# Kernel tuning notes

Hardware: AMD Instinct MI355X
Metric: run time of the kernel (lower is better)

The kernel has to match this reference:

```python
import jax, jax.numpy as jnp
import numpy as np

N, E, G = 50000, 800000, 200
F_IN, C, HEADS = 16, 64, 4
HID = C * HEADS  # 256


def setup_inputs() -> dict:
    key = jax.random.key(0)
    ks = jax.random.split(key, 30)
    rn = lambda k, s, sc=0.1: jax.random.normal(k, s, jnp.float32) * sc
    inp = {
        'x': jax.random.normal(ks[0], (N, F_IN), jnp.float32),
        'edge_index': jax.random.randint(ks[1], (2, E), 0, N, jnp.int32),
        'batch': jnp.sort(jax.random.randint(ks[2], (N,), 0, G, jnp.int32)),
        'Wl1': rn(ks[3], (F_IN, HID)), 'Wr1': rn(ks[4], (F_IN, HID)),
        'att1': rn(ks[5], (HEADS, C)), 'b1': rn(ks[6], (HID,)),
        'g1': jnp.ones((HID,), jnp.float32), 'be1': jnp.zeros((HID,), jnp.float32),
        'Wl2': rn(ks[7], (HID, HID)), 'Wr2': rn(ks[8], (HID, HID)),
        'att2': rn(ks[9], (HEADS, C)), 'b2': rn(ks[10], (HID,)),
        'g2': jnp.ones((HID,), jnp.float32), 'be2': jnp.zeros((HID,), jnp.float32),
        # GATv2 layer 3: 256 -> 64, 1 head, mean (concat=False)
        'Wl3': rn(ks[11], (HID, C)), 'Wr3': rn(ks[12], (HID, C)),
        'att3': rn(ks[13], (1, C)), 'b3': rn(ks[14], (C,)),
        'g3': jnp.ones((C,), jnp.float32), 'be3': jnp.zeros((C,), jnp.float32),
        # classifier MLP: 128 -> 64 -> 1
        'Wc1': rn(ks[15], (2 * C, C)), 'bc1': rn(ks[16], (C,)),
        'Wc2': rn(ks[17], (C, 1)), 'bc2': rn(ks[18], (1,)),
    }
    return inp


def _gatv2(x, src, dst, Wl, Wr, att, b, heads, c, concat):
    n = x.shape[0]
    xl = (x @ Wl).reshape(n, heads, c)
    xr = (x @ Wr).reshape(n, heads, c)
    s = jax.nn.leaky_relu(xl[src] + xr[dst], 0.2)       # [E', H, C]
    e = jnp.einsum('ehc,hc->eh', s, att)                 # [E', H]
    m = jax.ops.segment_max(e, dst, num_segments=n)
    p = jnp.exp(e - m[dst])
    denom = jax.ops.segment_sum(p, dst, num_segments=n)
    alpha = p / (denom[dst] + 1e-16)
    out = jax.ops.segment_sum(alpha[:, :, None] * xl[src], dst, num_segments=n)
    out = out.reshape(n, heads * c) if concat else out.mean(axis=1)
    return out + b


def _bn(x, g, b):
    mu = x.mean(0)
    v = x.var(0)
    return (x - mu) * jax.lax.rsqrt(v + 1e-5) * g + b


def reference(x, edge_index, batch,
              Wl1, Wr1, att1, b1, g1, be1,
              Wl2, Wr2, att2, b2, g2, be2,
              Wl3, Wr3, att3, b3, g3, be3,
              Wc1, bc1, Wc2, bc2):
    n = x.shape[0]
    loop = jnp.arange(n, dtype=edge_index.dtype)
    src = jnp.concatenate([edge_index[0], loop])  # PyG add_self_loops=True
    dst = jnp.concatenate([edge_index[1], loop])

    h = _gatv2(x, src, dst, Wl1, Wr1, att1, b1, HEADS, C, True)
    h = jax.nn.elu(_bn(h, g1, be1))  # dropout disabled (eval)
    h = _gatv2(h, src, dst, Wl2, Wr2, att2, b2, HEADS, C, True)
    h = jax.nn.elu(_bn(h, g2, be2))
    h = _gatv2(h, src, dst, Wl3, Wr3, att3, b3, 1, C, False)
    h = _bn(h, g3, be3)

    cnt = jax.ops.segment_sum(jnp.ones((n, 1), h.dtype), batch, num_segments=G)
    mean_pool = jax.ops.segment_sum(h, batch, num_segments=G) / jnp.maximum(cnt, 1.0)
    max_pool = jax.ops.segment_max(h, batch, num_segments=G)
    pooled = jnp.concatenate([mean_pool, max_pool], axis=1)  # [G, 128]

    out = jax.nn.relu(pooled @ Wc1 + bc1)
    out = out @ Wc2 + bc2  # [G, 1]
    return out
```

## Files before the change

kernel.cpp:

```cpp
#include <hip/hip_runtime.h>
#include <math.h>

#define N_NODES 50000
#define N_EDGES 800000
#define ET (N_EDGES + N_NODES)
#define N_GRAPHS 200
#define F_INN 16
#define C_DIM 64
#define N_HEADS 4
#define HIDD 256
#define SCAN_BLOCKS ((N_NODES + 255) / 256)

typedef __attribute__((ext_vector_type(8))) short short8;
typedef __attribute__((ext_vector_type(8))) ushort ushort8;
typedef __attribute__((ext_vector_type(4))) float f32x4;
typedef __attribute__((ext_vector_type(2))) float f32x2;

__device__ __forceinline__ float bf2f(ushort u) {
  return __uint_as_float(((unsigned)u) << 16);
}
__device__ __forceinline__ ushort f2bf(float f) {
  unsigned u = __float_as_uint(f);
  u += 0x7fff + ((u >> 16) & 1);
  return (ushort)(u >> 16);
}

__device__ __forceinline__ f32x2 emax2(f32x2 a, f32x2 b) {
#if __has_builtin(__builtin_elementwise_max)
  return __builtin_elementwise_max(a, b);
#else
  f32x2 r;
  r.x = fmaxf(a.x, b.x);
  r.y = fmaxf(a.y, b.y);
  return r;
#endif
}

template<int K, int M>
__global__ __launch_bounds__(256) void gemm_dual(
    const float* __restrict__ A, const float* __restrict__ Bl,
    const float* __restrict__ Br, ushort* __restrict__ Clb,
    ushort* __restrict__ Crb, int nrows)
{
  __shared__ __align__(16) float As[16][64];
  __shared__ __align__(16) float Bls[16][64];
  __shared__ __align__(16) float Brs[16][64];
  int tid = threadIdx.x;
  int row0 = blockIdx.x * 64;
  int col0 = blockIdx.y * 64;
  int tr = (tid >> 4) << 2;
  int tc = (tid & 15) << 2;
  float accL[4][4] = {{0.f}}, accR[4][4] = {{0.f}};
  int arow = tid >> 2, ak = (tid & 3) << 2;
  int brow = tid >> 4, bcol = (tid & 15) << 2;
  for (int k0 = 0; k0 < K; k0 += 16) {
    float4 av = make_float4(0.f, 0.f, 0.f, 0.f);
    int gr = row0 + arow;
    if (gr < nrows) av = *(const float4*)&A[(size_t)gr * K + k0 + ak];
    As[ak + 0][arow] = av.x;
    As[ak + 1][arow] = av.y;
    As[ak + 2][arow] = av.z;
    As[ak + 3][arow] = av.w;
    *(float4*)&Bls[brow][bcol] = *(const float4*)&Bl[(size_t)(k0 + brow) * M + col0 + bcol];
    *(float4*)&Brs[brow][bcol] = *(const float4*)&Br[(size_t)(k0 + brow) * M + col0 + bcol];
    __syncthreads();
    #pragma unroll
    for (int k = 0; k < 16; ++k) {
      float4 a = *(const float4*)&As[k][tr];
      float4 bl = *(const float4*)&Bls[k][tc];
      float4 br = *(const float4*)&Brs[k][tc];
      float aa[4] = {a.x, a.y, a.z, a.w};
      float lb[4] = {bl.x, bl.y, bl.z, bl.w};
      float rb[4] = {br.x, br.y, br.z, br.w};
      #pragma unroll
      for (int ii = 0; ii < 4; ++ii)
        #pragma unroll
        for (int jj = 0; jj < 4; ++jj) {
          accL[ii][jj] = fmaf(aa[ii], lb[jj], accL[ii][jj]);
          accR[ii][jj] = fmaf(aa[ii], rb[jj], accR[ii][jj]);
        }
    }
    __syncthreads();
  }
  #pragma unroll
  for (int ii = 0; ii < 4; ++ii) {
    int gr = row0 + tr + ii;
    if (gr < nrows) {
      *(ushort4*)&Clb[(size_t)gr * M + col0 + tc] =
          make_ushort4(f2bf(accL[ii][0]), f2bf(accL[ii][1]),
                       f2bf(accL[ii][2]), f2bf(accL[ii][3]));
      *(ushort4*)&Crb[(size_t)gr * M + col0 + tc] =
          make_ushort4(f2bf(accR[ii][0]), f2bf(accR[ii][1]),
                       f2bf(accR[ii][2]), f2bf(accR[ii][3]));
    }
  }
}

__device__ __forceinline__ void split_bf16(float a, ushort& hi, ushort& lo) {
  unsigned u = __float_as_uint(a);
  hi = (ushort)(u >> 16);
  float ah = __uint_as_float(u & 0xffff0000u);
  float r = a - ah;
  lo = (ushort)(__float_as_uint(r) >> 16);
}

template<int K, int N>
__global__ void convertB(const float* __restrict__ W, ushort* __restrict__ BTmat) {
  int idx = blockIdx.x * blockDim.x + threadIdx.x;
  if (idx >= K * N) return;
  int k = idx / N, n = idx - k * N;
  ushort hi, lo;
  split_bf16(W[idx], hi, lo);
  size_t dst = ((size_t)(k >> 3) * N + n) * 8 + (k & 7);
  BTmat[dst] = hi;
  BTmat[(size_t)(K / 8) * N * 8 + dst] = lo;
}

template<int N>
__global__ __launch_bounds__(N * 2) void gemm_fused(
    const float* __restrict__ H, const float* __restrict__ gsum,
    const float* __restrict__ gsumsq, const float* __restrict__ g,
    const float* __restrict__ be, const ushort* __restrict__ BT,
    ushort* __restrict__ Clb, ushort* __restrict__ Crb)
{
  constexpr int THREADS = N * 2;
  constexpr int PLANE = 32 * N * 8;
  __shared__ float SCs[256], SHs[256];
  __shared__ ushort Ah_s[64 * 256];
  __shared__ ushort Al_s[64 * 256];
  const int tid = threadIdx.x;
  const int brow0 = blockIdx.x * 64;

  const float invn = 1.0f / (float)N_NODES;
  for (int c = tid; c < 256; c += THREADS) {
    float mu = gsum[c] * invn;
    float var = gsumsq[c] * invn - mu * mu;
    float sc = g[c] * rsqrtf(var + 1e-5f);
    SCs[c] = sc;
    SHs[c] = be[c] - mu * sc;
  }
  __syncthreads();

  for (int gid = tid; gid < 2048; gid += THREADS) {
    int r = gid >> 5;
    int ch0 = (gid & 31) * 8;
    int grow = min(brow0 + r, N_NODES - 1);
    float4 v0 = *(const float4*)&H[(size_t)grow * 256 + ch0];
    float4 v1 = *(const float4*)&H[(size_t)grow * 256 + ch0 + 4];
    float4 sc0 = *(const float4*)&SCs[ch0];
    float4 sc1 = *(const float4*)&SCs[ch0 + 4];
    float4 sh0 = *(const float4*)&SHs[ch0];
    float4 sh1 = *(const float4*)&SHs[ch0 + 4];
    float vv[8] = {v0.x, v0.y, v0.z, v0.w, v1.x, v1.y, v1.z, v1.w};
    float scv[8] = {sc0.x, sc0.y, sc0.z, sc0.w, sc1.x, sc1.y, sc1.z, sc1.w};
    float shv[8] = {sh0.x, sh0.y, sh0.z, sh0.w, sh1.x, sh1.y, sh1.z, sh1.w};
    short8 hi8, lo8;
    #pragma unroll
    for (int j = 0; j < 8; ++j) {
      float t = fmaf(vv[j], scv[j], shv[j]);
      float e = t > 0.f ? t : __expf(t) - 1.f;
      ushort h, l;
      split_bf16(e, h, l);
      hi8[j] = (short)h;
      lo8[j] = (short)l;
    }
    int off = r * 512 + ((ch0 * 2) ^ ((r & 7) << 4));
    *(short8*)((char*)Ah_s + off) = hi8;
    *(short8*)((char*)Al_s + off) = lo8;
  }
  __syncthreads();

  const int wave = tid >> 6, lane = tid & 63;
  const int cn = lane & 15, kgrp = lane >> 4;
  const int combc = wave * 64;
  const bool isR = combc >= N;
  const ushort* Bh = BT + (isR ? 2 * PLANE : 0);
  const ushort* Bl_ = Bh + PLANE;
  const int cb = combc & (N - 1);
  f32x4 acc[4][4];
  #pragma unroll
  for (int rt = 0; rt < 4; ++rt)
    #pragma unroll
    for (int ct = 0; ct < 4; ++ct) acc[rt][ct] = (f32x4)(0.f);

  #pragma unroll 2
  for (int k0 = 0; k0 < 256; k0 += 32) {
    short8 ah[4], al[4];
    #pragma unroll
    for (int rt = 0; rt < 4; ++rt) {
      int row = rt * 16 + cn;
      int off = row * 512 + (((k0 * 2) + kgrp * 16) ^ ((row & 7) << 4));
      ah[rt] = *(const short8*)((const char*)Ah_s + off);
      al[rt] = *(const short8*)((const char*)Al_s + off);
    }
    const size_t bbase = (size_t)((k0 >> 3) + kgrp) * (N * 8);
    #pragma unroll
    for (int ct = 0; ct < 4; ++ct) {
      const size_t bo = bbase + (size_t)(cb + ct * 16 + cn) * 8;
      short8 bh = *(const short8*)&Bh[bo];
      short8 bl = *(const short8*)&Bl_[bo];
      #pragma unroll
      for (int rt = 0; rt < 4; ++rt) {
        acc[rt][ct] = __builtin_amdgcn_mfma_f32_16x16x32_bf16(ah[rt], bh, acc[rt][ct], 0, 0, 0);
        acc[rt][ct] = __builtin_amdgcn_mfma_f32_16x16x32_bf16(ah[rt], bl, acc[rt][ct], 0, 0, 0);
        acc[rt][ct] = __builtin_amdgcn_mfma_f32_16x16x32_bf16(al[rt], bh, acc[rt][ct], 0, 0, 0);
      }
    }
  }

  #pragma unroll
  for (int ct = 0; ct < 4; ++ct) {
    int cc = cb + ct * 16 + cn;
    #pragma unroll
    for (int rt = 0; rt < 4; ++rt) {
      int crow0 = brow0 + rt * 16 + kgrp * 4;
      #pragma unroll
      for (int j = 0; j < 4; ++j) {
        int rr = crow0 + j;
        if (rr < N_NODES) {
          if (!isR) Clb[(size_t)rr * N + cc] = f2bf(acc[rt][ct][j]);
          else      Crb[(size_t)rr * N + cc] = f2bf(acc[rt][ct][j]);
        }
      }
    }
  }
}

__global__ void hist_kernel(const int* __restrict__ dsts, int* __restrict__ curs) {
  int i = blockIdx.x * blockDim.x + threadIdx.x;
  if (i >= ET) return;
  int d = (i < N_EDGES) ? dsts[i] : i - N_EDGES;
  atomicAdd(&curs[d], 1);
}

__global__ __launch_bounds__(256) void scan_part(
    const int* __restrict__ curs, int* __restrict__ rows, int* __restrict__ bsum)
{
  __shared__ int tmp[256];
  int t = threadIdx.x;
  int i = blockIdx.x * 256 + t;
  int v = (i < N_NODES) ? curs[i] : 0;
  tmp[t] = v;
  __syncthreads();
  #pragma unroll
  for (int off = 1; off < 256; off <<= 1) {
    int u = (t >= off) ? tmp[t - off] : 0;
    __syncthreads();
    tmp[t] += u;
    __syncthreads();
  }
  if (i < N_NODES) rows[i] = tmp[t] - v;
  if (t == 255) bsum[blockIdx.x] = tmp[255];
}

__global__ __launch_bounds__(256) void scan_bsums(
    const int* __restrict__ bsum, int* __restrict__ boff)
{
  __shared__ int tmp[256];
  int t = threadIdx.x;
  int v = (t < SCAN_BLOCKS) ? bsum[t] : 0;
  tmp[t] = v;
  __syncthreads();
  #pragma unroll
  for (int off = 1; off < 256; off <<= 1) {
    int u = (t >= off) ? tmp[t - off] : 0;
    __syncthreads();
    tmp[t] += u;
    __syncthreads();
  }
  if (t < SCAN_BLOCKS) boff[t] = tmp[t] - v;
}

__global__ __launch_bounds__(256) void scan_apply(
    int* __restrict__ rows, const int* __restrict__ boff, int* __restrict__ curs)
{
  int i = blockIdx.x * 256 + threadIdx.x;
  if (i < N_NODES) {
    int r = rows[i] + boff[blockIdx.x];
    rows[i] = r;
    curs[i] = r;
  }
  if (i == 0) rows[N_NODES] = ET;
}

__global__ void scatter_kernel(const int* __restrict__ srcs, const int* __restrict__ dsts,
                               int* __restrict__ curs, int* __restrict__ esrc) {
  int i = blockIdx.x * blockDim.x + threadIdx.x;
  if (i >= ET) return;
  int s, d;
  if (i < N_EDGES) { s = srcs[i]; d = dsts[i]; } else { s = d = i - N_EDGES; }
  int pos = atomicAdd(&curs[d], 1);
  esrc[pos] = s;
}

__global__ __launch_bounds__(256) void flash256(
    const ushort* __restrict__ xl, const ushort* __restrict__ xr,
    const float* __restrict__ att, const int* __restrict__ rows,
    const int* __restrict__ esrc, float* __restrict__ out)
{
  int d = blockIdx.x * 4 + (threadIdx.x >> 6);
  if (d >= N_NODES) return;
  int lane = threadIdx.x & 63;
  int beg = rows[d], end = rows[d + 1];
  ushort4 ur = *(const ushort4*)&xr[(size_t)d * 256 + lane * 4];
  float xq0 = bf2f(ur.x), xq1 = bf2f(ur.y), xq2 = bf2f(ur.z), xq3 = bf2f(ur.w);
  float4 w = *(const float4*)&att[lane * 4];
  auto score = [&](float b0, float b1, float b2, float b3) {
    float v0 = b0 + xq0, v1 = b1 + xq1, v2 = b2 + xq2, v3 = b3 + xq3;
    v0 = v0 > 0.f ? v0 : 0.2f * v0;
    v1 = v1 > 0.f ? v1 : 0.2f * v1;
    v2 = v2 > 0.f ? v2 : 0.2f * v2;
    v3 = v3 > 0.f ? v3 : 0.2f * v3;
    return fmaf(v0, w.x, fmaf(v1, w.y, fmaf(v2, w.z, v3 * w.w)));
  };
  float m = -INFINITY, s = 0.f;
  float a0 = 0.f, a1 = 0.f, a2 = 0.f, a3 = 0.f;
  int p = beg;
  for (; p + 4 <= end; p += 4) {
    int s1 = esrc[p], s2 = esrc[p + 1], s3 = esrc[p + 2], s4 = esrc[p + 3];
    ushort4 u1 = *(const ushort4*)&xl[(size_t)s1 * 256 + lane * 4];
    ushort4 u2 = *(const ushort4*)&xl[(size_t)s2 * 256 + lane * 4];
    ushort4 u3 = *(const ushort4*)&xl[(size_t)s3 * 256 + lane * 4];
    ushort4 u4 = *(const ushort4*)&xl[(size_t)s4 * 256 + lane * 4];
    float b10 = bf2f(u1.x), b11 = bf2f(u1.y), b12 = bf2f(u1.z), b13 = bf2f(u1.w);
    float b20 = bf2f(u2.x), b21 = bf2f(u2.y), b22 = bf2f(u2.z), b23 = bf2f(u2.w);
    float b30 = bf2f(u3.x), b31 = bf2f(u3.y), b32 = bf2f(u3.z), b33 = bf2f(u3.w);
    float b40 = bf2f(u4.x), b41 = bf2f(u4.y), b42 = bf2f(u4.z), b43 = bf2f(u4.w);
    float e1 = score(b10, b11, b12, b13);
    float e2 = score(b20, b21, b22, b23);
    float e3 = score(b30, b31, b32, b33);
    float e4 = score(b40, b41, b42, b43);
    e1 += __shfl_xor(e1, 1); e2 += __shfl_xor(e2, 1);
    e3 += __shfl_xor(e3, 1); e4 += __shfl_xor(e4, 1);
    e1 += __shfl_xor(e1, 2); e2 += __shfl_xor(e2, 2);
    e3 += __shfl_xor(e3, 2); e4 += __shfl_xor(e4, 2);
    e1 += __shfl_xor(e1, 4); e2 += __shfl_xor(e2, 4);
    e3 += __shfl_xor(e3, 4); e4 += __shfl_xor(e4, 4);
    e1 += __shfl_xor(e1, 8); e2 += __shfl_xor(e2, 8);
    e3 += __shfl_xor(e3, 8); e4 += __shfl_xor(e4, 8);
    float mn = fmaxf(fmaxf(m, fmaxf(e1, e2)), fmaxf(e3, e4));
    float f = __expf(m - mn);
    float p1 = __expf(e1 - mn);
    float p2 = __expf(e2 - mn);
    float p3 = __expf(e3 - mn);
    float p4 = __expf(e4 - mn);
    s = s * f + ((p1 + p2) + (p3 + p4));
    a0 = fmaf(a0, f, fmaf(p1, b10, fmaf(p2, b20, fmaf(p3, b30, p4 * b40))));
    a1 = fmaf(a1, f, fmaf(p1, b11, fmaf(p2, b21, fmaf(p3, b31, p4 * b41))));
    a2 = fmaf(a2, f, fmaf(p1, b12, fmaf(p2, b22, fmaf(p3, b32, p4 * b42))));
    a3 = fmaf(a3, f, fmaf(p1, b13, fmaf(p2, b23, fmaf(p3, b33, p4 * b43))));
    m = mn;
  }
  for (; p < end; ++p) {
    int s1 = esrc[p];
    ushort4 u1 = *(const ushort4*)&xl[(size_t)s1 * 256 + lane * 4];
    float b10 = bf2f(u1.x), b11 = bf2f(u1.y), b12 = bf2f(u1.z), b13 = bf2f(u1.w);
    float e1 = score(b10, b11, b12, b13);
    e1 += __shfl_xor(e1, 1);
    e1 += __shfl_xor(e1, 2);
    e1 += __shfl_xor(e1, 4);
    e1 += __shfl_xor(e1, 8);
    float mn = fmaxf(m, e1);
    float f = __expf(m - mn);
    float p1 = __expf(e1 - mn);
    s = fmaf(s, f, p1);
    a0 = fmaf(a0, f, p1 * b10);
    a1 = fmaf(a1, f, p1 * b11);
    a2 = fmaf(a2, f, p1 * b12);
    a3 = fmaf(a3, f, p1 * b13);
    m = mn;
  }
  float inv = 1.f / (s + 1e-16f);
  *(float4*)&out[(size_t)d * 256 + lane * 4] =
      make_float4(a0 * inv, a1 * inv, a2 * inv, a3 * inv);
}

__global__ __launch_bounds__(256) void flash64(
    const ushort* __restrict__ xl, const ushort* __restrict__ xr,
    const float* __restrict__ att, const int* __restrict__ rows,
    const int* __restrict__ esrc, float* __restrict__ out)
{
  const int wave = threadIdx.x >> 6, lane = threadIdx.x & 63;
  const int di = lane >> 3, sl = lane & 7;
  const int d = blockIdx.x * 32 + wave * 8 + di;
  const bool valid = d < N_NODES;
  const int dc = valid ? d : N_NODES - 1;
  const int ch = sl * 8;
  ushort8 uxr = *(const ushort8*)&xr[(size_t)dc * 64 + ch];
  float4 wa = *(const float4*)&att[ch];
  float4 wb = *(const float4*)&att[ch + 4];
  f32x2 xr0 = {bf2f(uxr[0]), bf2f(uxr[1])}, xr1 = {bf2f(uxr[2]), bf2f(uxr[3])};
  f32x2 xr2 = {bf2f(uxr[4]), bf2f(uxr[5])}, xr3 = {bf2f(uxr[6]), bf2f(uxr[7])};
  f32x2 w0 = {wa.x, wa.y}, w1 = {wa.z, wa.w}, w2 = {wb.x, wb.y}, w3 = {wb.z, wb.w};
  int beg = rows[dc], end = rows[dc + 1];
  float m = -INFINITY, s = 0.f;
  f32x2 a0 = {0.f, 0.f}, a1 = {0.f, 0.f}, a2 = {0.f, 0.f}, a3 = {0.f, 0.f};

  auto loadb = [&](int src, f32x2 b[4]) {
    ushort8 u = *(const ushort8*)&xl[(size_t)src * 64 + ch];
    b[0] = f32x2{bf2f(u[0]), bf2f(u[1])};
    b[1] = f32x2{bf2f(u[2]), bf2f(u[3])};
    b[2] = f32x2{bf2f(u[4]), bf2f(u[5])};
    b[3] = f32x2{bf2f(u[6]), bf2f(u[7])};
  };
  auto scoreP = [&](const f32x2 b[4]) -> float {
    f32x2 v0 = b[0] + xr0, v1 = b[1] + xr1, v2 = b[2] + xr2, v3 = b[3] + xr3;
    v0 = emax2(v0, v0 * 0.2f);
    v1 = emax2(v1, v1 * 0.2f);
    v2 = emax2(v2, v2 * 0.2f);
    v3 = emax2(v3, v3 * 0.2f);
    f32x2 dd = (v0 * w0 + v1 * w1) + (v2 * w2 + v3 * w3);
    return dd.x + dd.y;
  };
  auto one_edge = [&](int src) {
    f32x2 b[4];
    loadb(src, b);
    float e = scoreP(b);
    e += __shfl_xor(e, 1);
    e += __shfl_xor(e, 2);
    e += __shfl_xor(e, 4);
    float mn = fmaxf(m, e);
    float f = __expf(m - mn);
    float pe = __expf(e - mn);
    s = s * f + pe;
    a0 = a0 * f + b[0] * pe;
    a1 = a1 * f + b[1] * pe;
    a2 = a2 * f + b[2] * pe;
    a3 = a3 * f + b[3] * pe;
    m = mn;
  };

  int p = beg;
  int hd = min(end, (beg + 3) & ~3);
  for (; p < hd; ++p) one_edge(esrc[p]);
  for (; p + 4 <= end; p += 4) {
    int4 sv = *(const int4*)&esrc[p];
    f32x2 b1[4], b2[4], b3[4], b4[4];
    loadb(sv.x, b1);
    loadb(sv.y, b2);
    loadb(sv.z, b3);
    loadb(sv.w, b4);
    float e1 = scoreP(b1);
    float e2 = scoreP(b2);
    float e3 = scoreP(b3);
    float e4 = scoreP(b4);
    e1 += __shfl_xor(e1, 1); e2 += __shfl_xor(e2, 1);
    e3 += __shfl_xor(e3, 1); e4 += __shfl_xor(e4, 1);
    e1 += __shfl_xor(e1, 2); e2 += __shfl_xor(e2, 2);
    e3 += __shfl_xor(e3, 2); e4 += __shfl_xor(e4, 2);
    e1 += __shfl_xor(e1, 4); e2 += __shfl_xor(e2, 4);
    e3 += __shfl_xor(e3, 4); e4 += __shfl_xor(e4, 4);
    float mn = fmaxf(fmaxf(m, fmaxf(e1, e2)), fmaxf(e3, e4));
    float f = __expf(m - mn);
    float p1 = __expf(e1 - mn);
    float p2 = __expf(e2 - mn);
    float p3 = __expf(e3 - mn);
    float p4 = __expf(e4 - mn);
    s = s * f + ((p1 + p2) + (p3 + p4));
    a0 = a0 * f + ((b1[0] * p1 + b2[0] * p2) + (b3[0] * p3 + b4[0] * p4));
    a1 = a1 * f + ((b1[1] * p1 + b2[1] * p2) + (b3[1] * p3 + b4[1] * p4));
    a2 = a2 * f + ((b1[2] * p1 + b2[2] * p2) + (b3[2] * p3 + b4[2] * p4));
    a3 = a3 * f + ((b1[3] * p1 + b2[3] * p2) + (b3[3] * p3 + b4[3] * p4));
    m = mn;
  }
  for (; p < end; ++p) one_edge(esrc[p]);

  if (valid) {
    float inv = 1.f / (s + 1e-16f);
    *(float4*)&out[(size_t)d * 64 + ch] =
        make_float4(a0.x * inv, a0.y * inv, a1.x * inv, a1.y * inv);
    *(float4*)&out[(size_t)d * 64 + ch + 4] =
        make_float4(a2.x * inv, a2.y * inv, a3.x * inv, a3.y * inv);
  }
}

template<int D_, int RPB>
__global__ __launch_bounds__(256) void bn_stats(const float* __restrict__ h,
    float* __restrict__ gsum, float* __restrict__ gsumsq, int nrows)
{
  constexpr int RG = 256 / D_;
  int c = threadIdx.x % D_;
  int rg = threadIdx.x / D_;
  int r0 = blockIdx.x * RPB;
  float s = 0.f, sq = 0.f;
  int rend = min(r0 + RPB, nrows);
  for (int r = r0 + rg; r < rend; r += RG) {
    float v = h[(size_t)r * D_ + c];
    s += v;
    sq = fmaf(v, v, sq);
  }
  atomicAdd(&gsum[c], s);
  atomicAdd(&gsumsq[c], sq);
}

__global__ __launch_bounds__(256) void pool_mlp(
    const float* __restrict__ h3, const int* __restrict__ batch,
    const float* __restrict__ gsum, const float* __restrict__ gsumsq,
    const float* __restrict__ g3, const float* __restrict__ be3,
    const float* __restrict__ Wc1, const float* __restrict__ bc1,
    const float* __restrict__ Wc2, const float* __restrict__ bc2,
    float* __restrict__ outp)
{
  int g = blockIdx.x;
  int t = threadIdx.x;
  int lane = t & 63, w = t >> 6;
  int lo, hi;
  {
    int a = 0, b = N_NODES;
    while (a < b) { int mid = (a + b) >> 1; if (batch[mid] < g) a = mid + 1; else b = mid; }
    lo = a;
    b = N_NODES;
    while (a < b) { int mid = (a + b) >> 1; if (batch[mid] < g + 1) a = mid + 1; else b = mid; }
    hi = a;
  }
  const float invn = 1.0f / (float)N_NODES;
  float mu = gsum[lane] * invn;
  float var = gsumsq[lane] * invn - mu * mu;
  float scl = g3[lane] * rsqrtf(var + 1e-5f);
  float shf = be3[lane] - mu * scl;
  float s = 0.f, mx = -INFINITY;
  for (int r = lo + w; r < hi; r += 4) {
    float v = fmaf(h3[(size_t)r * 64 + lane], scl, shf);
    s += v;
    mx = fmaxf(mx, v);
  }
  __shared__ float ssum[4][64];
  __shared__ float smax[4][64];
  __shared__ float pooled[128];
  ssum[w][lane] = s;
  smax[w][lane] = mx;
  __syncthreads();
  if (w == 0) {
    float tot = ssum[0][lane] + ssum[1][lane] + ssum[2][lane] + ssum[3][lane];
    float m4 = fmaxf(fmaxf(smax[0][lane], smax[1][lane]),
                     fmaxf(smax[2][lane], smax[3][lane]));
    float cnt = (float)(hi - lo);
    pooled[lane] = tot / fmaxf(cnt, 1.f);
    pooled[64 + lane] = m4;
  }
  __syncthreads();
  if (w == 0) {
    float a = bc1[lane];
    #pragma unroll 8
    for (int k = 0; k < 128; ++k) a = fmaf(pooled[k], Wc1[k * 64 + lane], a);
    a = fmaxf(a, 0.f);
    float v = a * Wc2[lane];
    v += __shfl_xor(v, 1);
    v += __shfl_xor(v, 2);
    v += __shfl_xor(v, 4);
    v += __shfl_xor(v, 8);
    v += __shfl_xor(v, 16);
    v += __shfl_xor(v, 32);
    if (lane == 0) outp[g] = v + bc2[0];
  }
}

extern "C" void kernel_launch(void* const* d_in, const int* in_sizes, int n_in,
                              void* d_out, int out_size, void* d_ws, size_t ws_size,
                              hipStream_t stream)
{
  const float* x    = (const float*)d_in[0];
  const int*   ei   = (const int*)d_in[1];
  const int*   batch= (const int*)d_in[2];
  const float* Wl1  = (const float*)d_in[3];
  const float* Wr1  = (const float*)d_in[4];
  const float* att1 = (const float*)d_in[5];
  const float* g1   = (const float*)d_in[7];
  const float* be1  = (const float*)d_in[8];
  const float* Wl2  = (const float*)d_in[9];
  const float* Wr2  = (const float*)d_in[10];
  const float* att2 = (const float*)d_in[11];
  const float* g2   = (const float*)d_in[13];
  const float* be2  = (const float*)d_in[14];
  const float* Wl3  = (const float*)d_in[15];
  const float* Wr3  = (const float*)d_in[16];
  const float* att3 = (const float*)d_in[17];
  const float* g3   = (const float*)d_in[19];
  const float* be3  = (const float*)d_in[20];
  const float* Wc1  = (const float*)d_in[21];
  const float* bc1  = (const float*)d_in[22];
  const float* Wc2  = (const float*)d_in[23];
  const float* bc2  = (const float*)d_in[24];

  const int* srcs = ei;
  const int* dsts = ei + N_EDGES;

  float* ws = (float*)d_ws;
  size_t o = 0;
  ushort* XLB = (ushort*)(ws + o); o += (size_t)N_NODES * HIDD / 2;
  ushort* XRB = (ushort*)(ws + o); o += (size_t)N_NODES * HIDD / 2;
  float* Hb = ws + o;            o += (size_t)N_NODES * HIDD;
  ushort* BT2 = (ushort*)(ws + o); o += (size_t)4 * 32 * 256 * 8 / 2;
  ushort* BT3 = (ushort*)(ws + o); o += (size_t)4 * 32 * 64 * 8 / 2;
  int* ESRC = (int*)(ws + o);    o += ET;
  int* ROWS = (int*)(ws + o);    o += N_NODES + 1;
  int* CURS = (int*)(ws + o);    o += N_NODES;
  int* BSUM = (int*)(ws + o);    o += SCAN_BLOCKS;
  int* BOFF = (int*)(ws + o);    o += SCAN_BLOCKS;
  float* GS  = ws + o;           o += 256;
  float* GSQ = ws + o;           o += 256;

  const int ROW_BLOCKS = (N_NODES + 63) / 64;
  const int DST_BLOCKS = (N_NODES + 3) / 4;
  constexpr int PLANE2 = 32 * 256 * 8;
  constexpr int PLANE3 = 32 * 64 * 8;

  convertB<256, 256><<<(65536 + 255) / 256, 256, 0, stream>>>(Wl2, BT2);
  convertB<256, 256><<<(65536 + 255) / 256, 256, 0, stream>>>(Wr2, BT2 + 2 * PLANE2);
  convertB<256, 64><<<(16384 + 255) / 256, 256, 0, stream>>>(Wl3, BT3);
  convertB<256, 64><<<(16384 + 255) / 256, 256, 0, stream>>>(Wr3, BT3 + 2 * PLANE3);

  hipMemsetAsync(CURS, 0, N_NODES * 4, stream);
  hist_kernel<<<(ET + 255) / 256, 256, 0, stream>>>(dsts, CURS);
  scan_part<<<SCAN_BLOCKS, 256, 0, stream>>>(CURS, ROWS, BSUM);
  scan_bsums<<<1, 256, 0, stream>>>(BSUM, BOFF);
  scan_apply<<<SCAN_BLOCKS, 256, 0, stream>>>(ROWS, BOFF, CURS);
  scatter_kernel<<<(ET + 255) / 256, 256, 0, stream>>>(srcs, dsts, CURS, ESRC);

  gemm_dual<16, 256><<<dim3(ROW_BLOCKS, 4), 256, 0, stream>>>(
      x, Wl1, Wr1, XLB, XRB, N_NODES);
  flash256<<<DST_BLOCKS, 256, 0, stream>>>(XLB, XRB, att1, ROWS, ESRC, Hb);
  hipMemsetAsync(GS, 0, 512 * 4, stream);
  bn_stats<256, 64><<<ROW_BLOCKS, 256, 0, stream>>>(Hb, GS, GSQ, N_NODES);

  gemm_fused<256><<<ROW_BLOCKS, 512, 0, stream>>>(
      Hb, GS, GSQ, g1, be1, BT2, XLB, XRB);
  flash256<<<DST_BLOCKS, 256, 0, stream>>>(XLB, XRB, att2, ROWS, ESRC, Hb);
  hipMemsetAsync(GS, 0, 512 * 4, stream);
  bn_stats<256, 64><<<ROW_BLOCKS, 256, 0, stream>>>(Hb, GS, GSQ, N_NODES);

  gemm_fused<64><<<ROW_BLOCKS, 128, 0, stream>>>(
      Hb, GS, GSQ, g2, be2, BT3, XLB, XRB);
  flash64<<<(N_NODES + 31) / 32, 256, 0, stream>>>(XLB, XRB, att3, ROWS, ESRC, Hb);
  hipMemsetAsync(GS, 0, 512 * 4, stream);
  bn_stats<64, 256><<<(N_NODES + 255) / 256, 256, 0, stream>>>(Hb, GS, GSQ, N_NODES);

  pool_mlp<<<N_GRAPHS, 256, 0, stream>>>(Hb, batch, GS, GSQ, g3, be3,
                                         Wc1, bc1, Wc2, bc2, (float*)d_out);
}
```

Measured before the change: 548.0 us.

## Degree-sort destination nodes, lazy softmax rescale, exp2, and smaller GEMM row tiles

Adds a counting sort of destination nodes by degree (descending), so each wave's attention kernel processes nodes with similar edge counts and work per block is more balanced. The online softmax now skips rescaling when no score in a batch of four exceeds the running max by more than a threshold, and it uses exp2 with the attention weights prescaled by log2(e). Gather offsets switch to 32-bit arithmetic. The fused GEMM tile shrinks from 64 to 32 rows per block, giving more blocks and less LDS per block. The cost is three extra small kernels and a scattered per-node access order.

```diff
diff --git a/kernel.cpp b/kernel.cpp
--- a/kernel.cpp
+++ b/kernel.cpp
@@ -16,6 +16,8 @@
 typedef __attribute__((ext_vector_type(4))) float f32x4;
 typedef __attribute__((ext_vector_type(2))) float f32x2;
 
+#define LOG2E 1.44269504088896340736f
+
 __device__ __forceinline__ float bf2f(ushort u) {
   return __uint_as_float(((unsigned)u) << 16);
 }
@@ -23,6 +25,13 @@
   unsigned u = __float_as_uint(f);
   u += 0x7fff + ((u >> 16) & 1);
   return (ushort)(u >> 16);
+}
+__device__ __forceinline__ float ex2(float x) {
+#if __has_builtin(__builtin_amdgcn_exp2f)
+  return __builtin_amdgcn_exp2f(x);
+#else
+  return exp2f(x);
+#endif
 }
 
 __device__ __forceinline__ f32x2 emax2(f32x2 a, f32x2 b) {
@@ -126,10 +135,10 @@
   constexpr int THREADS = N * 2;
   constexpr int PLANE = 32 * N * 8;
   __shared__ float SCs[256], SHs[256];
-  __shared__ ushort Ah_s[64 * 256];
-  __shared__ ushort Al_s[64 * 256];
+  __shared__ ushort Ah_s[32 * 256];
+  __shared__ ushort Al_s[32 * 256];
   const int tid = threadIdx.x;
-  const int brow0 = blockIdx.x * 64;
+  const int brow0 = blockIdx.x * 32;
 
   const float invn = 1.0f / (float)N_NODES;
   for (int c = tid; c < 256; c += THREADS) {
@@ -141,7 +150,7 @@
   }
   __syncthreads();
 
-  for (int gid = tid; gid < 2048; gid += THREADS) {
+  for (int gid = tid; gid < 1024; gid += THREADS) {
     int r = gid >> 5;
     int ch0 = (gid & 31) * 8;
     int grow = min(brow0 + r, N_NODES - 1);
@@ -177,17 +186,17 @@
   const ushort* Bh = BT + (isR ? 2 * PLANE : 0);
   const ushort* Bl_ = Bh + PLANE;
   const int cb = combc & (N - 1);
-  f32x4 acc[4][4];
+  f32x4 acc[2][4];
   #pragma unroll
-  for (int rt = 0; rt < 4; ++rt)
+  for (int rt = 0; rt < 2; ++rt)
     #pragma unroll
     for (int ct = 0; ct < 4; ++ct) acc[rt][ct] = (f32x4)(0.f);
 
   #pragma unroll 2
   for (int k0 = 0; k0 < 256; k0 += 32) {
-    short8 ah[4], al[4];
+    short8 ah[2], al[2];
     #pragma unroll
-    for (int rt = 0; rt < 4; ++rt) {
+    for (int rt = 0; rt < 2; ++rt) {
       int row = rt * 16 + cn;
       int off = row * 512 + (((k0 * 2) + kgrp * 16) ^ ((row & 7) << 4));
       ah[rt] = *(const short8*)((const char*)Ah_s + off);
@@ -200,7 +209,7 @@
       short8 bh = *(const short8*)&Bh[bo];
       short8 bl = *(const short8*)&Bl_[bo];
       #pragma unroll
-      for (int rt = 0; rt < 4; ++rt) {
+      for (int rt = 0; rt < 2; ++rt) {
         acc[rt][ct] = __builtin_amdgcn_mfma_f32_16x16x32_bf16(ah[rt], bh, acc[rt][ct], 0, 0, 0);
         acc[rt][ct] = __builtin_amdgcn_mfma_f32_16x16x32_bf16(ah[rt], bl, acc[rt][ct], 0, 0, 0);
         acc[rt][ct] = __builtin_amdgcn_mfma_f32_16x16x32_bf16(al[rt], bh, acc[rt][ct], 0, 0, 0);
@@ -212,7 +221,7 @@
   for (int ct = 0; ct < 4; ++ct) {
     int cc = cb + ct * 16 + cn;
     #pragma unroll
-    for (int rt = 0; rt < 4; ++rt) {
+    for (int rt = 0; rt < 2; ++rt) {
       int crow0 = brow0 + rt * 16 + kgrp * 4;
       #pragma unroll
       for (int j = 0; j < 4; ++j) {
@@ -293,18 +302,41 @@
   esrc[pos] = s;
 }
 
+__global__ void deg_hist_kernel(const int* __restrict__ rows, int* __restrict__ dhist) {
+  int i = blockIdx.x * blockDim.x + threadIdx.x;
+  if (i >= N_NODES) return;
+  int deg = rows[i + 1] - rows[i];
+  atomicAdd(&dhist[min(deg, 63)], 1);
+}
+__global__ void deg_scan_kernel(const int* __restrict__ dhist, int* __restrict__ doff) {
+  if (threadIdx.x == 0) {
+    int acc = 0;
+    for (int b = 63; b >= 0; --b) { doff[b] = acc; acc += dhist[b]; }
+  }
+}
+__global__ void deg_scatter_kernel(const int* __restrict__ rows, int* __restrict__ doff,
+                                   int* __restrict__ dord) {
+  int i = blockIdx.x * blockDim.x + threadIdx.x;
+  if (i >= N_NODES) return;
+  int deg = rows[i + 1] - rows[i];
+  int pos = atomicAdd(&doff[min(deg, 63)], 1);
+  dord[pos] = i;
+}
+
 __global__ __launch_bounds__(256) void flash256(
     const ushort* __restrict__ xl, const ushort* __restrict__ xr,
     const float* __restrict__ att, const int* __restrict__ rows,
-    const int* __restrict__ esrc, float* __restrict__ out)
-{
-  int d = blockIdx.x * 4 + (threadIdx.x >> 6);
-  if (d >= N_NODES) return;
-  int lane = threadIdx.x & 63;
+    const int* __restrict__ esrc, const int* __restrict__ dord,
+    float* __restrict__ out)
+{
+  const int wave = threadIdx.x >> 6, lane = threadIdx.x & 63;
+  const int d = dord[blockIdx.x * 4 + wave];
+  const unsigned lo4 = lane * 4;
   int beg = rows[d], end = rows[d + 1];
-  ushort4 ur = *(const ushort4*)&xr[(size_t)d * 256 + lane * 4];
+  ushort4 ur = *(const ushort4*)&xr[(size_t)d * 256 + lo4];
   float xq0 = bf2f(ur.x), xq1 = bf2f(ur.y), xq2 = bf2f(ur.z), xq3 = bf2f(ur.w);
-  float4 w = *(const float4*)&att[lane * 4];
+  float4 w = *(const float4*)&att[lo4];
+  w.x *= LOG2E; w.y *= LOG2E; w.z *= LOG2E; w.w *= LOG2E;
   auto score = [&](float b0, float b1, float b2, float b3) {
     float v0 = b0 + xq0, v1 = b1 + xq1, v2 = b2 + xq2, v3 = b3 + xq3;
     v0 = v0 > 0.f ? v0 : 0.2f * v0;
@@ -318,10 +350,14 @@
   int p = beg;
   for (; p + 4 <= end; p += 4) {
     int s1 = esrc[p], s2 = esrc[p + 1], s3 = esrc[p + 2], s4 = esrc[p + 3];
-    ushort4 u1 = *(const ushort4*)&xl[(size_t)s1 * 256 + lane * 4];
-    ushort4 u2 = *(const ushort4*)&xl[(size_t)s2 * 256 + lane * 4];
-    ushort4 u3 = *(const ushort4*)&xl[(size_t)s3 * 256 + lane * 4];
-    ushort4 u4 = *(const ushort4*)&xl[(size_t)s4 * 256 + lane * 4];
+    unsigned o1 = ((unsigned)s1 << 8) + lo4;
+    unsigned o2 = ((unsigned)s2 << 8) + lo4;
+    unsigned o3 = ((unsigned)s3 << 8) + lo4;
+    unsigned o4 = ((unsigned)s4 << 8) + lo4;
+    ushort4 u1 = *(const ushort4*)&xl[o1];
+    ushort4 u2 = *(const ushort4*)&xl[o2];
+    ushort4 u3 = *(const ushort4*)&xl[o3];
+    ushort4 u4 = *(const ushort4*)&xl[o4];
     float b10 = bf2f(u1.x), b11 = bf2f(u1.y), b12 = bf2f(u1.z), b13 = bf2f(u1.w);
     float b20 = bf2f(u2.x), b21 = bf2f(u2.y), b22 = bf2f(u2.z), b23 = bf2f(u2.w);
     float b30 = bf2f(u3.x), b31 = bf2f(u3.y), b32 = bf2f(u3.z), b33 = bf2f(u3.w);
@@ -338,22 +374,36 @@
     e3 += __shfl_xor(e3, 4); e4 += __shfl_xor(e4, 4);
     e1 += __shfl_xor(e1, 8); e2 += __shfl_xor(e2, 8);
     e3 += __shfl_xor(e3, 8); e4 += __shfl_xor(e4, 8);
-    float mn = fmaxf(fmaxf(m, fmaxf(e1, e2)), fmaxf(e3, e4));
-    float f = __expf(m - mn);
-    float p1 = __expf(e1 - mn);
-    float p2 = __expf(e2 - mn);
-    float p3 = __expf(e3 - mn);
-    float p4 = __expf(e4 - mn);
-    s = s * f + ((p1 + p2) + (p3 + p4));
-    a0 = fmaf(a0, f, fmaf(p1, b10, fmaf(p2, b20, fmaf(p3, b30, p4 * b40))));
-    a1 = fmaf(a1, f, fmaf(p1, b11, fmaf(p2, b21, fmaf(p3, b31, p4 * b41))));
-    a2 = fmaf(a2, f, fmaf(p1, b12, fmaf(p2, b22, fmaf(p3, b32, p4 * b42))));
-    a3 = fmaf(a3, f, fmaf(p1, b13, fmaf(p2, b23, fmaf(p3, b33, p4 * b43))));
-    m = mn;
+    float gm = fmaxf(fmaxf(e1, e2), fmaxf(e3, e4));
+    if (__all(gm <= m + 8.0f)) {
+      float p1 = ex2(e1 - m);
+      float p2 = ex2(e2 - m);
+      float p3 = ex2(e3 - m);
+      float p4 = ex2(e4 - m);
+      s += (p1 + p2) + (p3 + p4);
+      a0 = fmaf(p1, b10, fmaf(p2, b20, fmaf(p3, b30, fmaf(p4, b40, a0))));
+      a1 = fmaf(p1, b11, fmaf(p2, b21, fmaf(p3, b31, fmaf(p4, b41, a1))));
+      a2 = fmaf(p1, b12, fmaf(p2, b22, fmaf(p3, b32, fmaf(p4, b42, a2))));
+      a3 = fmaf(p1, b13, fmaf(p2, b23, fmaf(p3, b33, fmaf(p4, b43, a3))));
+    } else {
+      float mn = fmaxf(m, gm);
+      float f = ex2(m - mn);
+      float p1 = ex2(e1 - mn);
+      float p2 = ex2(e2 - mn);
+      float p3 = ex2(e3 - mn);
+      float p4 = ex2(e4 - mn);
+      s = s * f + ((p1 + p2) + (p3 + p4));
+      a0 = fmaf(a0, f, fmaf(p1, b10, fmaf(p2, b20, fmaf(p3, b30, p4 * b40))));
+      a1 = fmaf(a1, f, fmaf(p1, b11, fmaf(p2, b21, fmaf(p3, b31, p4 * b41))));
+      a2 = fmaf(a2, f, fmaf(p1, b12, fmaf(p2, b22, fmaf(p3, b32, p4 * b42))));
+      a3 = fmaf(a3, f, fmaf(p1, b13, fmaf(p2, b23, fmaf(p3, b33, p4 * b43))));
+      m = mn;
+    }
   }
   for (; p < end; ++p) {
     int s1 = esrc[p];
-    ushort4 u1 = *(const ushort4*)&xl[(size_t)s1 * 256 + lane * 4];
+    unsigned o1 = ((unsigned)s1 << 8) + lo4;
+    ushort4 u1 = *(const ushort4*)&xl[o1];
     float b10 = bf2f(u1.x), b11 = bf2f(u1.y), b12 = bf2f(u1.z), b13 = bf2f(u1.w);
     float e1 = score(b10, b11, b12, b13);
     e1 += __shfl_xor(e1, 1);
@@ -361,8 +411,8 @@
     e1 += __shfl_xor(e1, 4);
     e1 += __shfl_xor(e1, 8);
     float mn = fmaxf(m, e1);
-    float f = __expf(m - mn);
-    float p1 = __expf(e1 - mn);
+    float f = ex2(m - mn);
+    float p1 = ex2(e1 - mn);
     s = fmaf(s, f, p1);
     a0 = fmaf(a0, f, p1 * b10);
     a1 = fmaf(a1, f, p1 * b11);
@@ -371,33 +421,36 @@
     m = mn;
   }
   float inv = 1.f / (s + 1e-16f);
-  *(float4*)&out[(size_t)d * 256 + lane * 4] =
+  *(float4*)&out[(size_t)d * 256 + lo4] =
       make_float4(a0 * inv, a1 * inv, a2 * inv, a3 * inv);
 }
 
 __global__ __launch_bounds__(256) void flash64(
     const ushort* __restrict__ xl, const ushort* __restrict__ xr,
     const float* __restrict__ att, const int* __restrict__ rows,
-    const int* __restrict__ esrc, float* __restrict__ out)
+    const int* __restrict__ esrc, const int* __restrict__ dord,
+    float* __restrict__ out)
 {
   const int wave = threadIdx.x >> 6, lane = threadIdx.x & 63;
   const int di = lane >> 3, sl = lane & 7;
-  const int d = blockIdx.x * 32 + wave * 8 + di;
-  const bool valid = d < N_NODES;
-  const int dc = valid ? d : N_NODES - 1;
-  const int ch = sl * 8;
-  ushort8 uxr = *(const ushort8*)&xr[(size_t)dc * 64 + ch];
+  const int idx = blockIdx.x * 32 + wave * 8 + di;
+  const bool valid = idx < N_NODES;
+  const int d = dord[valid ? idx : 0];
+  const unsigned ch = sl * 8;
+  ushort8 uxr = *(const ushort8*)&xr[(size_t)d * 64 + ch];
   float4 wa = *(const float4*)&att[ch];
   float4 wb = *(const float4*)&att[ch + 4];
   f32x2 xr0 = {bf2f(uxr[0]), bf2f(uxr[1])}, xr1 = {bf2f(uxr[2]), bf2f(uxr[3])};
   f32x2 xr2 = {bf2f(uxr[4]), bf2f(uxr[5])}, xr3 = {bf2f(uxr[6]), bf2f(uxr[7])};
-  f32x2 w0 = {wa.x, wa.y}, w1 = {wa.z, wa.w}, w2 = {wb.x, wb.y}, w3 = {wb.z, wb.w};
-  int beg = rows[dc], end = rows[dc + 1];
+  f32x2 w0 = {wa.x * LOG2E, wa.y * LOG2E}, w1 = {wa.z * LOG2E, wa.w * LOG2E};
+  f32x2 w2 = {wb.x * LOG2E, wb.y * LOG2E}, w3 = {wb.z * LOG2E, wb.w * LOG2E};
+  int beg = rows[d], end = rows[d + 1];
   float m = -INFINITY, s = 0.f;
   f32x2 a0 = {0.f, 0.f}, a1 = {0.f, 0.f}, a2 = {0.f, 0.f}, a3 = {0.f, 0.f};
 
   auto loadb = [&](int src, f32x2 b[4]) {
-    ushort8 u = *(const ushort8*)&xl[(size_t)src * 64 + ch];
+    unsigned off = ((unsigned)src << 6) + ch;
+    ushort8 u = *(const ushort8*)&xl[off];
     b[0] = f32x2{bf2f(u[0]), bf2f(u[1])};
     b[1] = f32x2{bf2f(u[2]), bf2f(u[3])};
     b[2] = f32x2{bf2f(u[4]), bf2f(u[5])};
@@ -420,8 +473,8 @@
     e += __shfl_xor(e, 2);
     e += __shfl_xor(e, 4);
     float mn = fmaxf(m, e);
-    float f = __expf(m - mn);
-    float pe = __expf(e - mn);
+    float f = ex2(m - mn);
+    float pe = ex2(e - mn);
     s = s * f + pe;
     a0 = a0 * f + b[0] * pe;
     a1 = a1 * f + b[1] * pe;
@@ -450,18 +503,31 @@
     e3 += __shfl_xor(e3, 2); e4 += __shfl_xor(e4, 2);
     e1 += __shfl_xor(e1, 4); e2 += __shfl_xor(e2, 4);
     e3 += __shfl_xor(e3, 4); e4 += __shfl_xor(e4, 4);
-    float mn = fmaxf(fmaxf(m, fmaxf(e1, e2)), fmaxf(e3, e4));
-    float f = __expf(m - mn);
-    float p1 = __expf(e1 - mn);
-    float p2 = __expf(e2 - mn);
-    float p3 = __expf(e3 - mn);
-    float p4 = __expf(e4 - mn);
-    s = s * f + ((p1 + p2) + (p3 + p4));
-    a0 = a0 * f + ((b1[0] * p1 + b2[0] * p2) + (b3[0] * p3 + b4[0] * p4));
-    a1 = a1 * f + ((b1[1] * p1 + b2[1] * p2) + (b3[1] * p3 + b4[1] * p4));
-    a2 = a2 * f + ((b1[2] * p1 + b2[2] * p2) + (b3[2] * p3 + b4[2] * p4));
-    a3 = a3 * f + ((b1[3] * p1 + b2[3] * p2) + (b3[3] * p3 + b4[3] * p4));
-    m = mn;
+    float gm = fmaxf(fmaxf(e1, e2), fmaxf(e3, e4));
+    if (__all(gm <= m + 8.0f)) {
+      float p1 = ex2(e1 - m);
+      float p2 = ex2(e2 - m);
+      float p3 = ex2(e3 - m);
+      float p4 = ex2(e4 - m);
+      s += (p1 + p2) + (p3 + p4);
+      a0 = a0 + ((b1[0] * p1 + b2[0] * p2) + (b3[0] * p3 + b4[0] * p4));
+      a1 = a1 + ((b1[1] * p1 + b2[1] * p2) + (b3[1] * p3 + b4[1] * p4));
+      a2 = a2 + ((b1[2] * p1 + b2[2] * p2) + (b3[2] * p3 + b4[2] * p4));
+      a3 = a3 + ((b1[3] * p1 + b2[3] * p2) + (b3[3] * p3 + b4[3] * p4));
+    } else {
+      float mn = fmaxf(m, gm);
+      float f = ex2(m - mn);
+      float p1 = ex2(e1 - mn);
+      float p2 = ex2(e2 - mn);
+      float p3 = ex2(e3 - mn);
+      float p4 = ex2(e4 - mn);
+      s = s * f + ((p1 + p2) + (p3 + p4));
+      a0 = a0 * f + ((b1[0] * p1 + b2[0] * p2) + (b3[0] * p3 + b4[0] * p4));
+      a1 = a1 * f + ((b1[1] * p1 + b2[1] * p2) + (b3[1] * p3 + b4[1] * p4));
+      a2 = a2 * f + ((b1[2] * p1 + b2[2] * p2) + (b3[2] * p3 + b4[2] * p4));
+      a3 = a3 * f + ((b1[3] * p1 + b2[3] * p2) + (b3[3] * p3 + b4[3] * p4));
+      m = mn;
+    }
   }
   for (; p < end; ++p) one_edge(esrc[p]);
 
@@ -595,12 +661,16 @@
   int* ESRC = (int*)(ws + o);    o += ET;
   int* ROWS = (int*)(ws + o);    o += N_NODES + 1;
   int* CURS = (int*)(ws + o);    o += N_NODES;
+  int* DHIST = (int*)(ws + o);   o += 64;
+  int* DOFF = (int*)(ws + o);    o += 64;
+  int* DORD = (int*)(ws + o);    o += N_NODES;
   int* BSUM = (int*)(ws + o);    o += SCAN_BLOCKS;
   int* BOFF = (int*)(ws + o);    o += SCAN_BLOCKS;
   float* GS  = ws + o;           o += 256;
   float* GSQ = ws + o;           o += 256;
 
   const int ROW_BLOCKS = (N_NODES + 63) / 64;
+  const int ROW_BLOCKS32 = (N_NODES + 31) / 32;
   const int DST_BLOCKS = (N_NODES + 3) / 4;
   constexpr int PLANE2 = 32 * 256 * 8;
   constexpr int PLANE3 = 32 * 64 * 8;
@@ -610,28 +680,31 @@
   convertB<256, 64><<<(16384 + 255) / 256, 256, 0, stream>>>(Wl3, BT3);
   convertB<256, 64><<<(16384 + 255) / 256, 256, 0, stream>>>(Wr3, BT3 + 2 * PLANE3);
 
-  hipMemsetAsync(CURS, 0, N_NODES * 4, stream);
+  hipMemsetAsync(CURS, 0, (N_NODES + 64) * 4, stream);
   hist_kernel<<<(ET + 255) / 256, 256, 0, stream>>>(dsts, CURS);
   scan_part<<<SCAN_BLOCKS, 256, 0, stream>>>(CURS, ROWS, BSUM);
   scan_bsums<<<1, 256, 0, stream>>>(BSUM, BOFF);
   scan_apply<<<SCAN_BLOCKS, 256, 0, stream>>>(ROWS, BOFF, CURS);
   scatter_kernel<<<(ET + 255) / 256, 256, 0, stream>>>(srcs, dsts, CURS, ESRC);
+  deg_hist_kernel<<<SCAN_BLOCKS, 256, 0, stream>>>(ROWS, DHIST);
+  deg_scan_kernel<<<1, 64, 0, stream>>>(DHIST, DOFF);
+  deg_scatter_kernel<<<SCAN_BLOCKS, 256, 0, stream>>>(ROWS, DOFF, DORD);
 
   gemm_dual<16, 256><<<dim3(ROW_BLOCKS, 4), 256, 0, stream>>>(
       x, Wl1, Wr1, XLB, XRB, N_NODES);
-  flash256<<<DST_BLOCKS, 256, 0, stream>>>(XLB, XRB, att1, ROWS, ESRC, Hb);
+  flash256<<<DST_BLOCKS, 256, 0, stream>>>(XLB, XRB, att1, ROWS, ESRC, DORD, Hb);
   hipMemsetAsync(GS, 0, 512 * 4, stream);
   bn_stats<256, 64><<<ROW_BLOCKS, 256, 0, stream>>>(Hb, GS, GSQ, N_NODES);
 
-  gemm_fused<256><<<ROW_BLOCKS, 512, 0, stream>>>(
+  gemm_fused<256><<<ROW_BLOCKS32, 512, 0, stream>>>(
       Hb, GS, GSQ, g1, be1, BT2, XLB, XRB);
-  flash256<<<DST_BLOCKS, 256, 0, stream>>>(XLB, XRB, att2, ROWS, ESRC, Hb);
+  flash256<<<DST_BLOCKS, 256, 0, stream>>>(XLB, XRB, att2, ROWS, ESRC, DORD, Hb);
   hipMemsetAsync(GS, 0, 512 * 4, stream);
   bn_stats<256, 64><<<ROW_BLOCKS, 256, 0, stream>>>(Hb, GS, GSQ, N_NODES);
 
-  gemm_fused<64><<<ROW_BLOCKS, 128, 0, stream>>>(
+  gemm_fused<64><<<ROW_BLOCKS32, 128, 0, stream>>>(
       Hb, GS, GSQ, g2, be2, BT3, XLB, XRB);
-  flash64<<<(N_NODES + 31) / 32, 256, 0, stream>>>(XLB, XRB, att3, ROWS, ESRC, Hb);
+  flash64<<<(N_NODES + 31) / 32, 256, 0, stream>>>(XLB, XRB, att3, ROWS, ESRC, DORD, Hb);
   hipMemsetAsync(GS, 0, 512 * 4, stream);
   bn_stats<64, 256><<<(N_NODES + 255) / 256, 256, 0, stream>>>(Hb, GS, GSQ, N_NODES);
 
```

New measurement: 801.8 us. +46.3%, slower.
